# Kernel tuning notes

Hardware: AMD Instinct MI355X
Metric: run time of the kernel (lower is better)

Reference implementation:

```python
import jax, jax.numpy as jnp
import numpy as np

B, S, D = 2, 2048, 4096
NQ, NKV, DK = 32, 4, 128
GROUPS = NQ // NKV  # 8
NEG = -1e9  # finite stand-in for -inf so fully-masked rows stay NaN-free


def setup_inputs() -> dict:
    key = jax.random.key(0)
    ks = jax.random.split(key, 5)
    return {
        "x": jax.random.normal(ks[0], (B, S, D), jnp.float32),
        "Wq": jax.random.normal(ks[1], (D, NQ * DK), jnp.float32) * 0.02,
        "Wk": jax.random.normal(ks[2], (D, NKV * DK), jnp.float32) * 0.02,
        "Wv": jax.random.normal(ks[3], (D, NKV * DK), jnp.float32) * 0.02,
        "Wo": jax.random.normal(ks[4], (NQ * DK, D), jnp.float32) * 0.02,
    }


def reference(x, Wq, Wk, Wv, Wo):
    b, s, _ = x.shape
    # projections -> [b, heads, s, dk]
    Q = (x @ Wq).reshape(b, s, NQ, DK).transpose(0, 2, 1, 3)
    K = (x @ Wk).reshape(b, s, NKV, DK).transpose(0, 2, 1, 3)
    V = (x @ Wv).reshape(b, s, NKV, DK).transpose(0, 2, 1, 3)
    # GQA: repeat_interleave KV heads to match Q heads
    K = jnp.repeat(K, GROUPS, axis=1)  # [b, NQ, s, dk]
    V = jnp.repeat(V, GROUPS, axis=1)
    scores = jnp.einsum("bhqd,bhkd->bhqk", Q, K) / np.sqrt(DK).astype(np.float32)
    # faithful to source: mask = triu(ones(s, kv_len), diag=kv_len-s+1); fill where mask==0
    mask = jnp.triu(jnp.ones((s, s), jnp.float32), k=1)
    scores = jnp.where(mask == 0, NEG, scores)
    attn = jax.nn.softmax(scores, axis=-1)  # dropout = identity (eval)
    out = jnp.einsum("bhqk,bhkd->bhqd", attn, V)
    out = out.transpose(0, 2, 1, 3).reshape(b, s, NQ * DK)
    return out @ Wo
```

## Files before the change

kernel.cpp:

```cpp
#include <hip/hip_runtime.h>
#include <hip/hip_bf16.h>

#define S_LEN 2048
#define DMODEL 4096
#define NQH 32
#define NKVH 4
#define DKH 128

typedef __attribute__((ext_vector_type(8))) short bf16x8;
typedef __attribute__((ext_vector_type(4))) float f32x4;

union PU { unsigned u[4]; bf16x8 v; };

__device__ __forceinline__ float b2f(short u) {
  union { float f; unsigned int i; } cv;
  cv.i = ((unsigned int)(unsigned short)u) << 16;
  return cv.f;
}

__device__ __forceinline__ unsigned cvt_pk(float lo, float hi) {
  unsigned r;
  asm("v_cvt_pk_bf16_f32 %0, %1, %2" : "=v"(r) : "v"(lo), "v"(hi));
  return r;
}

__device__ __forceinline__ void gload16(const void* g, void* l) {
  __builtin_amdgcn_global_load_lds(
      (const __attribute__((address_space(1))) void*)g,
      (__attribute__((address_space(3))) void*)l, 16, 0, 0);
}

#define BAR()                         \
  {                                   \
    asm volatile("" ::: "memory");    \
    __builtin_amdgcn_s_barrier();     \
    asm volatile("" ::: "memory");    \
  }

__global__ __launch_bounds__(256) void cast_kernel(
    const float* __restrict__ in, __hip_bfloat16* __restrict__ out, int n4) {
  for (int i = blockIdx.x * 256 + threadIdx.x; i < n4; i += gridDim.x * 256) {
    const float4 v = reinterpret_cast<const float4*>(in)[i];
    __hip_bfloat16 t[4] = {__float2bfloat16(v.x), __float2bfloat16(v.y),
                           __float2bfloat16(v.z), __float2bfloat16(v.w)};
    reinterpret_cast<uint2*>(out)[i] = *reinterpret_cast<const uint2*>(t);
  }
}

__global__ __launch_bounds__(256) void transpose_cast_kernel(
    const float* __restrict__ W, __hip_bfloat16* __restrict__ WT, int K, int N) {
  __shared__ __align__(16) __hip_bfloat16 tile[64][64];
  const int tid = threadIdx.x;
  const int n0 = blockIdx.x * 64, k0 = blockIdx.y * 64;
#pragma unroll
  for (int i = 0; i < 2; ++i) {
    const int fid = i * 256 + tid;
    const int r = fid >> 3, cc = fid & 7;
    const float4 v0 = *reinterpret_cast<const float4*>(
        &W[(size_t)(k0 + r) * N + n0 + cc * 8]);
    const float4 v1 = *reinterpret_cast<const float4*>(
        &W[(size_t)(k0 + r) * N + n0 + cc * 8 + 4]);
    __hip_bfloat16 t[8] = {__float2bfloat16(v0.x), __float2bfloat16(v0.y),
                           __float2bfloat16(v0.z), __float2bfloat16(v0.w),
                           __float2bfloat16(v1.x), __float2bfloat16(v1.y),
                           __float2bfloat16(v1.z), __float2bfloat16(v1.w)};
    *reinterpret_cast<bf16x8*>(&tile[r][(cc ^ (r & 7)) << 3]) =
        *reinterpret_cast<const bf16x8*>(t);
  }
  __syncthreads();
  const int n = tid >> 2, kw = tid & 3;
#pragma unroll
  for (int i = 0; i < 2; ++i) {
    const int kc = kw + i * 4;
    __hip_bfloat16 t[8];
#pragma unroll
    for (int j = 0; j < 8; ++j) {
      const int r = kc * 8 + j;
      t[j] = tile[r][((((n >> 3) ^ (r & 7)) << 3)) + (n & 7)];
    }
    *reinterpret_cast<bf16x8*>(&WT[(size_t)(n0 + n) * K + k0 + kc * 8]) =
        *reinterpret_cast<const bf16x8*>(t);
  }
}

template <int WMODE>
__global__ __launch_bounds__(512, 2) void gemm256(
    const __hip_bfloat16* __restrict__ A, const __hip_bfloat16* __restrict__ BT,
    void* __restrict__ C) {
  __shared__ __align__(16) char ldsA[131072];
  const char* lds = &ldsA[0];
  const int tid = threadIdx.x, lane = tid & 63, w = tid >> 6;
  const int l15 = lane & 15, g = lane >> 4;
  const int wr = w >> 2, wcn = w & 3;
  const int id = blockIdx.x;
  const int swz = (id & 7) * 32 + (id >> 3);
  const int bm = (swz >> 4) * 256, bn = (swz & 15) * 256;
  const int row0 = tid >> 3;
  const int kbg = ((tid & 7) * 16) ^ ((row0 & 7) << 4);
  const char* Ab = (const char*)A;
  const char* Bb = (const char*)BT;
  const size_t aR = (size_t)(bm + row0) * 8192 + kbg;
  const size_t bR = (size_t)(bn + row0) * 8192 + kbg;
  char* ldsw = const_cast<char*>(lds) + w * 1024;
  const int sw = (l15 & 7) << 4;
  const int okk = (g * 16) ^ sw;
  const int rA = (wr * 64 + l15) * 128;
  const int rB = (wcn * 32 + l15) * 128;

  f32x4 acc[8][4] = {};

#define STG2(XR, XB, DST)            \
  gload16(XB + (XR), ldsw + (DST));  \
  gload16(XB + (XR) + 524288, ldsw + (DST) + 8192)

  STG2(aR, Ab, 0);
  STG2(bR, Bb, 65536);
  STG2(aR + 1048576, Ab, 16384);
  STG2(bR + 1048576, Bb, 65536 + 16384);
  STG2(aR + 128, Ab, 32768);
  STG2(bR + 128, Bb, 65536 + 32768);

  for (int t = 0; t < 64; ++t) {
    const int pc = t & 1, pn = pc ^ 1;
    const int pA = pc * 32768, pB = 65536 + pc * 32768;
    const size_t s01 = (size_t)((t + 1 < 64) ? t + 1 : t - 1) * 128;
    const size_t s23 = (size_t)((t + 2 < 64) ? t + 2 : t) * 128;
    asm volatile("s_waitcnt vmcnt(4)" ::: "memory");
    BAR();
    bf16x8 a0[4][2], b0[2][2];
#pragma unroll
    for (int m = 0; m < 4; ++m)
#pragma unroll
      for (int kk = 0; kk < 2; ++kk)
        a0[m][kk] = *reinterpret_cast<const bf16x8*>(
            lds + pA + rA + m * 2048 + (okk ^ (kk << 6)));
#pragma unroll
    for (int n = 0; n < 2; ++n)
#pragma unroll
      for (int kk = 0; kk < 2; ++kk)
        b0[n][kk] = *reinterpret_cast<const bf16x8*>(
            lds + pB + rB + n * 2048 + (okk ^ (kk << 6)));
    STG2(aR + 1048576 + s01, Ab, pn * 32768 + 16384);
    BAR();
    __builtin_amdgcn_s_setprio(1);
#pragma unroll
    for (int kk = 0; kk < 2; ++kk)
#pragma unroll
      for (int m = 0; m < 4; ++m)
#pragma unroll
        for (int n = 0; n < 2; ++n)
          acc[m][n] = __builtin_amdgcn_mfma_f32_16x16x32_bf16(
              a0[m][kk], b0[n][kk], acc[m][n], 0, 0, 0);
    __builtin_amdgcn_s_setprio(0);
    bf16x8 b1[2][2];
#pragma unroll
    for (int n = 0; n < 2; ++n)
#pragma unroll
      for (int kk = 0; kk < 2; ++kk)
        b1[n][kk] = *reinterpret_cast<const bf16x8*>(
            lds + pB + 16384 + rB + n * 2048 + (okk ^ (kk << 6)));
    STG2(bR + 1048576 + s01, Bb, 65536 + pn * 32768 + 16384);
    BAR();
    __builtin_amdgcn_s_setprio(1);
#pragma unroll
    for (int kk = 0; kk < 2; ++kk)
#pragma unroll
      for (int m = 0; m < 4; ++m)
#pragma unroll
        for (int n = 0; n < 2; ++n)
          acc[m][2 + n] = __builtin_amdgcn_mfma_f32_16x16x32_bf16(
              a0[m][kk], b1[n][kk], acc[m][2 + n], 0, 0, 0);
    __builtin_amdgcn_s_setprio(0);
    bf16x8 a1[4][2];
#pragma unroll
    for (int m = 0; m < 4; ++m)
#pragma unroll
      for (int kk = 0; kk < 2; ++kk)
        a1[m][kk] = *reinterpret_cast<const bf16x8*>(
            lds + pA + 16384 + rA + m * 2048 + (okk ^ (kk << 6)));
    STG2(aR + s23, Ab, pc * 32768);
    BAR();
    __builtin_amdgcn_s_setprio(1);
#pragma unroll
    for (int kk = 0; kk < 2; ++kk)
#pragma unroll
      for (int m = 0; m < 4; ++m)
#pragma unroll
        for (int n = 0; n < 2; ++n)
          acc[4 + m][n] = __builtin_amdgcn_mfma_f32_16x16x32_bf16(
              a1[m][kk], b0[n][kk], acc[4 + m][n], 0, 0, 0);
    __builtin_amdgcn_s_setprio(0);
    STG2(bR + s23, Bb, 65536 + pc * 32768);
    __builtin_amdgcn_s_setprio(1);
#pragma unroll
    for (int kk = 0; kk < 2; ++kk)
#pragma unroll
      for (int m = 0; m < 4; ++m)
#pragma unroll
        for (int n = 0; n < 2; ++n)
          acc[4 + m][2 + n] = __builtin_amdgcn_mfma_f32_16x16x32_bf16(
              a1[m][kk], b1[n][kk], acc[4 + m][2 + n], 0, 0, 0);
    __builtin_amdgcn_s_setprio(0);
  }
  asm volatile("s_waitcnt vmcnt(0)" ::: "memory");

  const int crow0 = bm + wr * 64 + g * 4;
  const int ccol0 = bn + wcn * 32 + l15;
#pragma unroll
  for (int M = 0; M < 8; ++M)
#pragma unroll
    for (int N = 0; N < 4; ++N) {
      const int row = crow0 + (M >> 2) * 128 + (M & 3) * 16;
      const int col = ccol0 + (N >> 1) * 128 + (N & 1) * 16;
#pragma unroll
      for (int r = 0; r < 4; ++r) {
        if constexpr (WMODE == 0)
          ((float*)C)[(size_t)(row + r) * 4096 + col] = acc[M][N][r];
        else
          ((__hip_bfloat16*)C)[(size_t)(row + r) * 4096 + col] =
              __float2bfloat16(acc[M][N][r]);
      }
    }
}

__global__ __launch_bounds__(256) void gemm_kv(
    const __hip_bfloat16* __restrict__ A, const __hip_bfloat16* __restrict__ BT,
    __hip_bfloat16* __restrict__ Kb, __hip_bfloat16* __restrict__ VT, int M,
    int N, int K) {
  __shared__ __align__(16) __hip_bfloat16 As[128 * 32];
  __shared__ __align__(16) __hip_bfloat16 Bs[128 * 32];
  const int tid = threadIdx.x, lane = tid & 63, w = tid >> 6;
  const int l15 = lane & 15, l4 = lane >> 4;
  const int bm = blockIdx.y * 128, bn = blockIdx.x * 128;
  const int wr = (w >> 1) * 64, wc = (w & 1) * 64;
  const int srow = lane >> 2, scol = (lane & 3) * 8;
  const __hip_bfloat16* ga = &A[(size_t)(bm + w * 16 + srow) * K + scol];
  const __hip_bfloat16* gb = &BT[(size_t)(bn + w * 16 + srow) * K + scol];
  __hip_bfloat16* la0 = &As[w * 512];
  __hip_bfloat16* la1 = &As[(w + 4) * 512];
  __hip_bfloat16* lb0 = &Bs[w * 512];
  __hip_bfloat16* lb1 = &Bs[(w + 4) * 512];
  f32x4 acc[4][4] = {};

  for (int k0 = 0; k0 < K; k0 += 32) {
    gload16(ga, la0);
    gload16(ga + (size_t)64 * K, la1);
    gload16(gb, lb0);
    gload16(gb + (size_t)64 * K, lb1);
    ga += 32;
    gb += 32;
    __syncthreads();
    bf16x8 af[4], bfr[4];
#pragma unroll
    for (int m = 0; m < 4; ++m)
      af[m] = *reinterpret_cast<const bf16x8*>(
          &As[(wr + m * 16 + l15) * 32 + l4 * 8]);
#pragma unroll
    for (int n = 0; n < 4; ++n)
      bfr[n] = *reinterpret_cast<const bf16x8*>(
          &Bs[(wc + n * 16 + l15) * 32 + l4 * 8]);
#pragma unroll
    for (int m = 0; m < 4; ++m)
#pragma unroll
      for (int n = 0; n < 4; ++n)
        acc[m][n] = __builtin_amdgcn_mfma_f32_16x16x32_bf16(af[m], bfr[n],
                                                            acc[m][n], 0, 0, 0);
    __syncthreads();
  }

#pragma unroll
  for (int m = 0; m < 4; ++m)
#pragma unroll
    for (int n = 0; n < 4; ++n)
#pragma unroll
      for (int r = 0; r < 4; ++r) {
        const int row = bm + wr + m * 16 + l4 * 4 + r;
        const int col = bn + wc + n * 16 + l15;
        if (col < 512) {
          Kb[(size_t)row * 512 + col] = __float2bfloat16(acc[m][n][r]);
        } else {
          const int b = row >> 11, s = row & 2047;
          VT[(size_t)(b * 512 + (col - 512)) * 2048 + s] =
              __float2bfloat16(acc[m][n][r]);
        }
      }
}

__global__ __launch_bounds__(512, 4) void attn_kernel(
    const __hip_bfloat16* __restrict__ Q, const __hip_bfloat16* __restrict__ Kb,
    const __hip_bfloat16* __restrict__ VT, __hip_bfloat16* __restrict__ O) {
  __shared__ __align__(16) __hip_bfloat16 Kbuf[2][64 * 128];
  __shared__ __align__(16) __hip_bfloat16 Vbuf[2][128 * 64];
  const int tid = threadIdx.x, lane = tid & 63, w = tid >> 6;
  const int l15 = lane & 15, g = (lane >> 4) & 3;
  const int d = blockIdx.x;
  const int xg = d & 7, hh = (d >> 3) & 7, pr = d >> 6;
  const int bh = xg * 8 + hh;
  const int b = bh >> 5, h = bh & 31, kvh = (bh & 31) >> 3;
  const char* kbase = (const char*)Kb + (size_t)(b * S_LEN) * 1024 + kvh * 256;
  const char* vbase = (const char*)VT + (size_t)(b * 512 + kvh * 128) * 4096;
  const __hip_bfloat16* qbase =
      Q + (size_t)(b * S_LEN) * DMODEL + (size_t)h * DKH;
  __hip_bfloat16* obase = O + (size_t)(b * S_LEN) * DMODEL + (size_t)h * DKH;
  const int krr = lane >> 4, kcb = (lane & 15) * 16;
  const int vrr = lane >> 3, vcb = (lane & 7) * 16;
  char* klds = (char*)&Kbuf[0][0] + w * 2048;
  char* vlds = (char*)&Vbuf[0][0] + w * 2048;
  const int swr = (l15 & 7) * 16;
  const int sl_lo = l15 + ((g & 1) << 5);
  const int sl_hi = sl_lo + 16;
  const bool hi = (g & 2) != 0;
  const float SCL2 = 0.12751742f;

  int par = 0;
  for (int ph = 0; ph < 2; ++ph) {
    const int pp = ph ? (15 - pr) : pr;
    const int qw = pp * 128 + w * 16;
    const int qa = qw + l15;
    bf16x8 qf[4];
#pragma unroll
    for (int kb = 0; kb < 4; ++kb)
      qf[kb] = *reinterpret_cast<const bf16x8*>(
          &qbase[(size_t)(qw + l15) * DMODEL + kb * 32 + g * 8]);
    float lsum = 0.f;
    f32x4 oacc[8] = {};
    const int t0 = pp * 2;
    {
      const int kv0 = t0 * 64;
#pragma unroll
      for (int i = 0; i < 2; ++i) {
        const int rr = 8 * w + 4 * i + krr;
        gload16(kbase + (size_t)(kv0 + rr) * 1024 + (kcb ^ ((rr & 7) * 16)),
                klds + par * 16384 + i * 1024);
        const int r2 = 16 * w + 8 * i + vrr;
        gload16(vbase + (size_t)r2 * 4096 + kv0 * 2 + (vcb ^ ((r2 & 7) * 16)),
                vlds + par * 16384 + i * 1024);
      }
    }
    for (int t = t0; t < 32; ++t) {
      __syncthreads();
      if (t + 1 < 32) {
        const int kv0 = (t + 1) * 64;
        const int np = par ^ 1;
#pragma unroll
        for (int i = 0; i < 2; ++i) {
          const int rr = 8 * w + 4 * i + krr;
          gload16(kbase + (size_t)(kv0 + rr) * 1024 + (kcb ^ ((rr & 7) * 16)),
                  klds + np * 16384 + i * 1024);
          const int r2 = 16 * w + 8 * i + vrr;
          gload16(vbase + (size_t)r2 * 4096 + kv0 * 2 + (vcb ^ ((r2 & 7) * 16)),
                  vlds + np * 16384 + i * 1024);
        }
      }
      const char* kp = (const char*)&Kbuf[0][0] + par * 16384;
      const char* vp = (const char*)&Vbuf[0][0] + par * 16384;
      f32x4 sT[4];
#pragma unroll
      for (int c = 0; c < 4; ++c) {
        f32x4 s = {};
#pragma unroll
        for (int kb = 0; kb < 4; ++kb) {
          const bf16x8 kf = *reinterpret_cast<const bf16x8*>(
              kp + (16 * c + l15) * 256 + ((kb * 64 + g * 16) ^ swr));
          s = __builtin_amdgcn_mfma_f32_16x16x32_bf16(kf, qf[kb], s, 0, 0, 0);
        }
        sT[c] = s;
      }
      const int dthr = qa - t * 64 - 4 * g;
#pragma unroll
      for (int c = 0; c < 4; ++c)
#pragma unroll
        for (int r = 0; r < 4; ++r) {
          const float e =
              (16 * c + r > dthr)
                  ? __builtin_amdgcn_exp2f(fmaf(sT[c][r], SCL2, -16.f))
                  : 0.f;
          sT[c][r] = e;
          lsum += e;
        }
      unsigned P0[4], P1[4];
#pragma unroll
      for (int c = 0; c < 4; ++c) {
        P0[c] = cvt_pk(sT[c][0], sT[c][1]);
        P1[c] = cvt_pk(sT[c][2], sT[c][3]);
      }
#pragma unroll
      for (int ks = 0; ks < 2; ++ks) {
        const int a0 = (int)P0[2 * ks], a1 = (int)P1[2 * ks];
        const int b0 = (int)P0[2 * ks + 1], b1 = (int)P1[2 * ks + 1];
        const unsigned s0a = __shfl(a0, sl_lo), s0b = __shfl(b0, sl_lo);
        const unsigned s1a = __shfl(a1, sl_lo), s1b = __shfl(b1, sl_lo);
        const unsigned s2a = __shfl(a0, sl_hi), s2b = __shfl(b0, sl_hi);
        const unsigned s3a = __shfl(a1, sl_hi), s3b = __shfl(b1, sl_hi);
        PU pu;
        pu.u[0] = hi ? s0b : s0a;
        pu.u[1] = hi ? s1b : s1a;
        pu.u[2] = hi ? s2b : s2a;
        pu.u[3] = hi ? s3b : s3a;
#pragma unroll
        for (int n = 0; n < 8; ++n) {
          const bf16x8 vf = *reinterpret_cast<const bf16x8*>(
              vp + (16 * n + l15) * 128 + ((ks * 64 + g * 16) ^ swr));
          oacc[n] =
              __builtin_amdgcn_mfma_f32_16x16x32_bf16(vf, pu.v, oacc[n], 0, 0, 0);
        }
      }
      par ^= 1;
    }
    lsum += __shfl_xor(lsum, 16);
    lsum += __shfl_xor(lsum, 32);
    const float rinv = 1.f / lsum;
    __hip_bfloat16* orow = obase + (size_t)(qw + l15) * DMODEL;
#pragma unroll
    for (int n = 0; n < 8; ++n) {
      uint2 st;
      st.x = cvt_pk(oacc[n][0] * rinv, oacc[n][1] * rinv);
      st.y = cvt_pk(oacc[n][2] * rinv, oacc[n][3] * rinv);
      *reinterpret_cast<uint2*>(&orow[16 * n + 4 * g]) = st;
    }
    __syncthreads();
  }
}

__global__ __launch_bounds__(128) void fixup_kernel(
    const __hip_bfloat16* __restrict__ VT, __hip_bfloat16* __restrict__ O) {
  const int b = blockIdx.x >> 5;
  const int h = blockIdx.x & 31;
  const int kvh = h >> 3;
  const int dk = threadIdx.x;
  const __hip_bfloat16* row = &VT[(size_t)(b * 512 + kvh * DKH + dk) * S_LEN];
  float s = 0.f;
  for (int i = 0; i < S_LEN / 8; ++i) {
    const bf16x8 v = *reinterpret_cast<const bf16x8*>(&row[i * 8]);
#pragma unroll
    for (int j = 0; j < 8; ++j) s += b2f(v[j]);
  }
  O[(size_t)(b * S_LEN + S_LEN - 1) * DMODEL + h * DKH + dk] =
      __float2bfloat16(s * (1.f / S_LEN));
}

extern "C" void kernel_launch(void* const* d_in, const int* in_sizes, int n_in,
                              void* d_out, int out_size, void* d_ws,
                              size_t ws_size, hipStream_t stream) {
  (void)in_sizes; (void)n_in; (void)out_size; (void)ws_size;
  const float* x = (const float*)d_in[0];
  const float* Wq = (const float*)d_in[1];
  const float* Wk = (const float*)d_in[2];
  const float* Wv = (const float*)d_in[3];
  const float* Wo = (const float*)d_in[4];
  float* out = (float*)d_out;

  char* ws = (char*)d_ws;
  __hip_bfloat16* xb  = (__hip_bfloat16*)(ws + 0);
  __hip_bfloat16* WT0 = (__hip_bfloat16*)(ws + 33554432ull);
  __hip_bfloat16* KVT = (__hip_bfloat16*)(ws + 67108864ull);
  __hip_bfloat16* Qb  = (__hip_bfloat16*)(ws + 75497472ull);
  __hip_bfloat16* Kb  = (__hip_bfloat16*)(ws + 109051904ull);
  __hip_bfloat16* VT  = (__hip_bfloat16*)(ws + 113246208ull);
  __hip_bfloat16* AO  = xb;

  const int M = 2 * S_LEN;
  dim3 blk(256);

  cast_kernel<<<dim3(2048), blk, 0, stream>>>(x, xb, (M * DMODEL) / 4);
  transpose_cast_kernel<<<dim3(64, 64), blk, 0, stream>>>(Wq, WT0, DMODEL, DMODEL);
  gemm256<1><<<dim3(256), dim3(512), 0, stream>>>(xb, WT0, Qb);
  transpose_cast_kernel<<<dim3(8, 64), blk, 0, stream>>>(Wk, KVT, DMODEL, 512);
  transpose_cast_kernel<<<dim3(8, 64), blk, 0, stream>>>(Wv, KVT + 512ull * DMODEL, DMODEL, 512);
  gemm_kv<<<dim3(8, 32), blk, 0, stream>>>(xb, KVT, Kb, VT, M, 1024, DMODEL);
  attn_kernel<<<dim3(512), dim3(512), 0, stream>>>(Qb, Kb, VT, AO);
  fixup_kernel<<<dim3(64), dim3(128), 0, stream>>>(VT, AO);
  transpose_cast_kernel<<<dim3(64, 64), blk, 0, stream>>>(Wo, WT0, DMODEL, DMODEL);
  gemm256<0><<<dim3(256), dim3(512), 0, stream>>>(AO, WT0, out);
}
```

Before: 498.9 us.

## Fuse Q/K/V projections into one wide GEMM and hoist causal mask check

Concatenates transposed Wq, Wk and Wv into one weight buffer and computes Q, K and V^T with a single gemm256 launch over 320 tiles. The epilogue routes columns to the Q, K or transposed-V outputs, which removes the slower separate 128-tile gemm_kv kernel and its extra pass over x. The attention inner loop now computes exp unconditionally and applies the causal zeroing only for the first two diagonal-adjacent tiles, which cuts per-element compares on fully unmasked tiles. It also relies on 320 blocks mapping cleanly through the new swizzle, and it grows the transposed weight region to 5120 rows in the workspace.

New measurement: 510.9 us. 1.02x slower.

```diff
diff --git a/kernel.cpp b/kernel.cpp
--- a/kernel.cpp
+++ b/kernel.cpp
@@ -83,18 +83,18 @@
   }
 }
 
-template <int WMODE>
+template <int WMODE, int NBN>
 __global__ __launch_bounds__(512, 2) void gemm256(
     const __hip_bfloat16* __restrict__ A, const __hip_bfloat16* __restrict__ BT,
-    void* __restrict__ C) {
+    void* __restrict__ C0, void* __restrict__ C1, void* __restrict__ C2) {
   __shared__ __align__(16) char ldsA[131072];
   const char* lds = &ldsA[0];
   const int tid = threadIdx.x, lane = tid & 63, w = tid >> 6;
   const int l15 = lane & 15, g = lane >> 4;
   const int wr = w >> 2, wcn = w & 3;
   const int id = blockIdx.x;
-  const int swz = (id & 7) * 32 + (id >> 3);
-  const int bm = (swz >> 4) * 256, bn = (swz & 15) * 256;
+  const int swz = (id & 7) * (2 * NBN) + (id >> 3);
+  const int bm = (swz / NBN) * 256, bn = (swz % NBN) * 256;
   const int row0 = tid >> 3;
   const int kbg = ((tid & 7) * 16) ^ ((row0 & 7) << 4);
   const char* Ab = (const char*)A;
@@ -214,76 +214,22 @@
       const int col = ccol0 + (N >> 1) * 128 + (N & 1) * 16;
 #pragma unroll
       for (int r = 0; r < 4; ++r) {
-        if constexpr (WMODE == 0)
-          ((float*)C)[(size_t)(row + r) * 4096 + col] = acc[M][N][r];
-        else
-          ((__hip_bfloat16*)C)[(size_t)(row + r) * 4096 + col] =
-              __float2bfloat16(acc[M][N][r]);
+        if constexpr (WMODE == 0) {
+          ((float*)C0)[(size_t)(row + r) * 4096 + col] = acc[M][N][r];
+        } else {
+          const __hip_bfloat16 v = __float2bfloat16(acc[M][N][r]);
+          if (col < 4096) {
+            ((__hip_bfloat16*)C0)[(size_t)(row + r) * 4096 + col] = v;
+          } else if (col < 4608) {
+            ((__hip_bfloat16*)C1)[(size_t)(row + r) * 512 + (col - 4096)] = v;
+          } else {
+            const int b = (row + r) >> 11, s = (row + r) & 2047;
+            ((__hip_bfloat16*)C2)[(size_t)(b * 512 + (col - 4608)) * 2048 + s] =
+                v;
+          }
+        }
       }
     }
-}
-
-__global__ __launch_bounds__(256) void gemm_kv(
-    const __hip_bfloat16* __restrict__ A, const __hip_bfloat16* __restrict__ BT,
-    __hip_bfloat16* __restrict__ Kb, __hip_bfloat16* __restrict__ VT, int M,
-    int N, int K) {
-  __shared__ __align__(16) __hip_bfloat16 As[128 * 32];
-  __shared__ __align__(16) __hip_bfloat16 Bs[128 * 32];
-  const int tid = threadIdx.x, lane = tid & 63, w = tid >> 6;
-  const int l15 = lane & 15, l4 = lane >> 4;
-  const int bm = blockIdx.y * 128, bn = blockIdx.x * 128;
-  const int wr = (w >> 1) * 64, wc = (w & 1) * 64;
-  const int srow = lane >> 2, scol = (lane & 3) * 8;
-  const __hip_bfloat16* ga = &A[(size_t)(bm + w * 16 + srow) * K + scol];
-  const __hip_bfloat16* gb = &BT[(size_t)(bn + w * 16 + srow) * K + scol];
-  __hip_bfloat16* la0 = &As[w * 512];
-  __hip_bfloat16* la1 = &As[(w + 4) * 512];
-  __hip_bfloat16* lb0 = &Bs[w * 512];
-  __hip_bfloat16* lb1 = &Bs[(w + 4) * 512];
-  f32x4 acc[4][4] = {};
-
-  for (int k0 = 0; k0 < K; k0 += 32) {
-    gload16(ga, la0);
-    gload16(ga + (size_t)64 * K, la1);
-    gload16(gb, lb0);
-    gload16(gb + (size_t)64 * K, lb1);
-    ga += 32;
-    gb += 32;
-    __syncthreads();
-    bf16x8 af[4], bfr[4];
-#pragma unroll
-    for (int m = 0; m < 4; ++m)
-      af[m] = *reinterpret_cast<const bf16x8*>(
-          &As[(wr + m * 16 + l15) * 32 + l4 * 8]);
-#pragma unroll
-    for (int n = 0; n < 4; ++n)
-      bfr[n] = *reinterpret_cast<const bf16x8*>(
-          &Bs[(wc + n * 16 + l15) * 32 + l4 * 8]);
-#pragma unroll
-    for (int m = 0; m < 4; ++m)
-#pragma unroll
-      for (int n = 0; n < 4; ++n)
-        acc[m][n] = __builtin_amdgcn_mfma_f32_16x16x32_bf16(af[m], bfr[n],
-                                                            acc[m][n], 0, 0, 0);
-    __syncthreads();
-  }
-
-#pragma unroll
-  for (int m = 0; m < 4; ++m)
-#pragma unroll
-    for (int n = 0; n < 4; ++n)
-#pragma unroll
-      for (int r = 0; r < 4; ++r) {
-        const int row = bm + wr + m * 16 + l4 * 4 + r;
-        const int col = bn + wc + n * 16 + l15;
-        if (col < 512) {
-          Kb[(size_t)row * 512 + col] = __float2bfloat16(acc[m][n][r]);
-        } else {
-          const int b = row >> 11, s = row & 2047;
-          VT[(size_t)(b * 512 + (col - 512)) * 2048 + s] =
-              __float2bfloat16(acc[m][n][r]);
-        }
-      }
 }
 
 __global__ __launch_bounds__(512, 4) void attn_kernel(
@@ -366,18 +312,23 @@
         }
         sT[c] = s;
       }
-      const int dthr = qa - t * 64 - 4 * g;
 #pragma unroll
       for (int c = 0; c < 4; ++c)
 #pragma unroll
-        for (int r = 0; r < 4; ++r) {
-          const float e =
-              (16 * c + r > dthr)
-                  ? __builtin_amdgcn_exp2f(fmaf(sT[c][r], SCL2, -16.f))
-                  : 0.f;
-          sT[c][r] = e;
-          lsum += e;
-        }
+        for (int r = 0; r < 4; ++r)
+          sT[c][r] = __builtin_amdgcn_exp2f(fmaf(sT[c][r], SCL2, -16.f));
+      if (t < t0 + 2) {
+        const int dthr = qa - t * 64 - 4 * g;
+#pragma unroll
+        for (int c = 0; c < 4; ++c)
+#pragma unroll
+          for (int r = 0; r < 4; ++r)
+            if (16 * c + r <= dthr) sT[c][r] = 0.f;
+      }
+#pragma unroll
+      for (int c = 0; c < 4; ++c)
+#pragma unroll
+        for (int r = 0; r < 4; ++r) lsum += sT[c][r];
       unsigned P0[4], P1[4];
 #pragma unroll
       for (int c = 0; c < 4; ++c) {
@@ -451,25 +402,27 @@
   float* out = (float*)d_out;
 
   char* ws = (char*)d_ws;
-  __hip_bfloat16* xb  = (__hip_bfloat16*)(ws + 0);
-  __hip_bfloat16* WT0 = (__hip_bfloat16*)(ws + 33554432ull);
-  __hip_bfloat16* KVT = (__hip_bfloat16*)(ws + 67108864ull);
-  __hip_bfloat16* Qb  = (__hip_bfloat16*)(ws + 75497472ull);
-  __hip_bfloat16* Kb  = (__hip_bfloat16*)(ws + 109051904ull);
-  __hip_bfloat16* VT  = (__hip_bfloat16*)(ws + 113246208ull);
-  __hip_bfloat16* AO  = xb;
+  __hip_bfloat16* xb    = (__hip_bfloat16*)(ws + 0);
+  __hip_bfloat16* WQKVT = (__hip_bfloat16*)(ws + 33554432ull);
+  __hip_bfloat16* Qb    = (__hip_bfloat16*)(ws + 75497472ull);
+  __hip_bfloat16* Kb    = (__hip_bfloat16*)(ws + 109051904ull);
+  __hip_bfloat16* VT    = (__hip_bfloat16*)(ws + 113246208ull);
+  __hip_bfloat16* AO    = xb;
+  __hip_bfloat16* WoT   = WQKVT;
 
   const int M = 2 * S_LEN;
   dim3 blk(256);
 
   cast_kernel<<<dim3(2048), blk, 0, stream>>>(x, xb, (M * DMODEL) / 4);
-  transpose_cast_kernel<<<dim3(64, 64), blk, 0, stream>>>(Wq, WT0, DMODEL, DMODEL);
-  gemm256<1><<<dim3(256), dim3(512), 0, stream>>>(xb, WT0, Qb);
-  transpose_cast_kernel<<<dim3(8, 64), blk, 0, stream>>>(Wk, KVT, DMODEL, 512);
-  transpose_cast_kernel<<<dim3(8, 64), blk, 0, stream>>>(Wv, KVT + 512ull * DMODEL, DMODEL, 512);
-  gemm_kv<<<dim3(8, 32), blk, 0, stream>>>(xb, KVT, Kb, VT, M, 1024, DMODEL);
+  transpose_cast_kernel<<<dim3(64, 64), blk, 0, stream>>>(Wq, WQKVT, DMODEL, DMODEL);
+  transpose_cast_kernel<<<dim3(8, 64), blk, 0, stream>>>(
+      Wk, WQKVT + 4096ull * 4096, DMODEL, 512);
+  transpose_cast_kernel<<<dim3(8, 64), blk, 0, stream>>>(
+      Wv, WQKVT + 4608ull * 4096, DMODEL, 512);
+  gemm256<2, 20><<<dim3(320), dim3(512), 0, stream>>>(xb, WQKVT, Qb, Kb, VT);
   attn_kernel<<<dim3(512), dim3(512), 0, stream>>>(Qb, Kb, VT, AO);
   fixup_kernel<<<dim3(64), dim3(128), 0, stream>>>(VT, AO);
-  transpose_cast_kernel<<<dim3(64, 64), blk, 0, stream>>>(Wo, WT0, DMODEL, DMODEL);
-  gemm256<0><<<dim3(256), dim3(512), 0, stream>>>(AO, WT0, out);
-}
+  transpose_cast_kernel<<<dim3(64, 64), blk, 0, stream>>>(Wo, WoT, DMODEL, DMODEL);
+  gemm256<0, 16><<<dim3(256), dim3(512), 0, stream>>>(AO, WoT, out, nullptr,
+                                                      nullptr);
+}
```
